# Performance work log

Hardware: AMD Instinct MI355X
Metric: run time of the kernel (lower is better)

## Reference

```python
import jax, jax.numpy as jnp
import numpy as np

N = 100000
E = 1600000
F_IN = 100
HID = 128
CLS = 47


def _glorot(key, shape):
    fan_in, fan_out = shape[1], shape[0]
    lim = (6.0 / (fan_in + fan_out)) ** 0.5
    return jax.random.uniform(key, shape, jnp.float32, -lim, lim)


def setup_inputs() -> dict:
    key = jax.random.key(0)
    ks = jax.random.split(key, 12)
    x0 = jax.random.normal(ks[0], (N, F_IN), jnp.float32)
    edge_index = jax.random.randint(ks[1], (2, E), 0, N, jnp.int32)
    edge_weight = jax.random.uniform(ks[2], (E,), jnp.float32)
    params = {
        'W1_rel': _glorot(ks[3], (HID, F_IN)),
        'W1_root': _glorot(ks[4], (HID, F_IN)),
        'b1': jnp.zeros((HID,), jnp.float32),
        'W2_rel': _glorot(ks[5], (HID, HID)),
        'W2_root': _glorot(ks[6], (HID, HID)),
        'b2': jnp.zeros((HID,), jnp.float32),
        'W3_rel': _glorot(ks[7], (HID, HID)),
        'W3_root': _glorot(ks[8], (HID, HID)),
        'b3': jnp.zeros((HID,), jnp.float32),
        'W_lin': _glorot(ks[9], (CLS, 3 * HID)),
        'b_lin': jnp.zeros((CLS,), jnp.float32),
    }
    return dict(x0=x0, edge_index=edge_index, edge_weight=edge_weight, **params)


def _graph_conv(x, src, dst, ew, W_rel, W_root, b):
    # gather source features, scale by edge weight, scatter-add to destinations
    msg = x[src] * ew[:, None]                       # [E, d]
    agg = jax.ops.segment_sum(msg, dst, num_segments=N)  # [N, d]
    return agg @ W_rel.T + x @ W_root.T + b


def reference(x0, edge_index, edge_weight,
              W1_rel, W1_root, b1,
              W2_rel, W2_root, b2,
              W3_rel, W3_root, b3,
              W_lin, b_lin):
    src, dst = edge_index[0], edge_index[1]
    x1 = jax.nn.relu(_graph_conv(x0, src, dst, edge_weight, W1_rel, W1_root, b1))
    x2 = jax.nn.relu(_graph_conv(x1, src, dst, edge_weight, W2_rel, W2_root, b2))
    x3 = jax.nn.relu(_graph_conv(x2, src, dst, edge_weight, W3_rel, W3_root, b3))
    x = jnp.concatenate([x1, x2, x3], axis=-1)       # [N, 3*HID]
    logits = x @ W_lin.T + b_lin                     # [N, CLS]
    return jax.nn.log_softmax(logits, axis=-1)
```

## Files before the change

### kernel.cpp

```cpp
#include <hip/hip_runtime.h>
#include <hip/hip_bf16.h>
#include <stdint.h>

#define NN 100000
#define NE 1600000
#define FIN 100
#define HID 128
#define CLS 47
#define NBUK 391
#define BCAP 4992

typedef __attribute__((ext_vector_type(8))) short bf16x8;
typedef __attribute__((ext_vector_type(4))) float f32x4;
typedef __attribute__((ext_vector_type(2))) float f32x2;

#define AS1(p) ((const __attribute__((address_space(1))) void*)(p))
#define AS3(p) ((__attribute__((address_space(3))) void*)(p))

__device__ __forceinline__ uint16_t f2bf(float f) {
  union { float f; uint32_t u; } v; v.f = f;
  uint32_t r = v.u + 0x7fffu + ((v.u >> 16) & 1u);
  return (uint16_t)(r >> 16);
}

__global__ void pack_weights(const float* __restrict__ W1r, const float* __restrict__ W1o,
                             const float* __restrict__ W2r, const float* __restrict__ W2o,
                             const float* __restrict__ W3r, const float* __restrict__ W3o,
                             uint16_t* __restrict__ B1, uint16_t* __restrict__ B2, uint16_t* __restrict__ B3) {
  int idx = blockIdx.x * 256 + threadIdx.x;
  int l = idx >> 15;
  int rem = idx & 32767;
  int j = rem >> 8;
  int k = rem & 255;
  if (l == 0) {
    uint16_t v = 0;
    if (k < FIN) v = f2bf(W1r[j*FIN + k]);
    else if (k >= 128 && k < 128 + FIN) v = f2bf(W1o[j*FIN + (k - 128)]);
    B1[j*256 + k] = v;
  } else if (l == 1) {
    B2[j*256 + k] = (k < 128) ? f2bf(W2r[j*128 + k]) : f2bf(W2o[j*128 + (k - 128)]);
  } else {
    B3[j*256 + k] = (k < 128) ? f2bf(W3r[j*128 + k]) : f2bf(W3o[j*128 + (k - 128)]);
  }
}

__global__ void pack_wl(const float* __restrict__ Wl, uint16_t* __restrict__ Wlb) {
  int idx = blockIdx.x * 256 + threadIdx.x;
  int r = idx / 384;
  int c = idx - r * 384;
  Wlb[idx] = (r < CLS) ? f2bf(Wl[r*384 + c]) : (uint16_t)0;
}

__global__ __launch_bounds__(256) void pad_x0(const float* __restrict__ x0, uint16_t* __restrict__ x0p,
                                              uint8_t* __restrict__ x0f8) {
  int n = blockIdx.x * 4 + (threadIdx.x >> 6);
  int c = 2 * (threadIdx.x & 63);
  uint32_t o = 0;
  uint16_t o8 = 0;
  if (c < FIN) {
    float2 v = *(const float2*)(x0 + (size_t)n*FIN + c);
    o = ((uint32_t)f2bf(v.y) << 16) | (uint32_t)f2bf(v.x);
    o8 = (uint16_t)__builtin_amdgcn_cvt_pk_fp8_f32(v.x, v.y, 0, false);
  }
  *(uint32_t*)(x0p + (size_t)n*HID + c) = o;
  *(uint16_t*)(x0f8 + (size_t)n*128 + c) = o8;
}

__global__ void binit(int* __restrict__ bfill) {
  int i = blockIdx.x * 256 + threadIdx.x;
  if (i < NBUK) bfill[i] = i * BCAP;
}

__global__ __launch_bounds__(512) void binscat(const int* __restrict__ src, const int* __restrict__ dst,
                                               const float* __restrict__ ew,
                                               int* __restrict__ bfill, int2* __restrict__ ebin) {
  __shared__ int h[NBUK];
  __shared__ int base[NBUK];
  int tid = threadIdx.x;
  for (int i = tid; i < NBUK; i += 512) h[i] = 0;
  __syncthreads();
  int tile0 = blockIdx.x * 8192;
  int n = NE - tile0; if (n > 8192) n = 8192;
  for (int i = tid; i < n; i += 512) atomicAdd(&h[dst[tile0 + i] >> 8], 1);
  __syncthreads();
  for (int i = tid; i < NBUK; i += 512) base[i] = h[i] ? atomicAdd(&bfill[i], h[i]) : 0;
  __syncthreads();
  for (int i = tid; i < NBUK; i += 512) h[i] = 0;
  __syncthreads();
  for (int i = tid; i < n; i += 512) {
    int e = tile0 + i;
    int d = dst[e];
    int b = d >> 8;
    int r = atomicAdd(&h[b], 1);
    ebin[base[b] + r] = make_int2(src[e] | ((d & 255) << 17), __float_as_int(ew[e]));
  }
}

__global__ __launch_bounds__(256) void bucket_csr(const int2* __restrict__ ebin,
                                                  const int* __restrict__ bfill,
                                                  int2* __restrict__ row_desc,
                                                  int2* __restrict__ erec) {
  __shared__ int sh[256];
  __shared__ int fill[256];
  __shared__ int cnt2s;
  int b = blockIdx.x;
  int tid = threadIdx.x;
  int base = b * BCAP;
  int cnt = bfill[b] - base;
  sh[tid] = 0;
  __syncthreads();
  for (int i = tid; i < cnt; i += 256) atomicAdd(&sh[(uint32_t)ebin[base + i].x >> 17], 1);
  __syncthreads();
  int histv = sh[tid];
  int hist2 = (histv + 1) & ~1;
  __syncthreads();
  sh[tid] = hist2;
  __syncthreads();
  for (int off = 1; off < 256; off <<= 1) {
    int tv = (tid >= off) ? sh[tid - off] : 0;
    __syncthreads();
    sh[tid] += tv;
    __syncthreads();
  }
  int excl2 = sh[tid] - hist2;
  if (tid == 255) cnt2s = sh[255];
  int node = b * 256 + tid;
  if (node < NN) row_desc[node] = make_int2(base + excl2, histv);
  fill[tid] = base + excl2;
  if (histv & 1) erec[base + excl2 + histv] = make_int2(0, 0);
  __syncthreads();
  for (int i = tid; i < cnt; i += 256) {
    int2 rec = ebin[base + i];
    int dl = (uint32_t)rec.x >> 17;
    int s = rec.x & 0x1FFFF;
    int pos = atomicAdd(&fill[dl], 1);
    erec[pos] = make_int2(s << 7, rec.y);
  }
  if (tid < 16) {
    int p = cnt2s + tid;
    if (p < BCAP) erec[base + p] = make_int2(0, 0);
  }
}

__global__ __launch_bounds__(256) void spmm_kernel(const uint8_t* __restrict__ x8,
                                                   const int2* __restrict__ row_desc,
                                                   const int2* __restrict__ erec,
                                                   uint16_t* __restrict__ agg) {
  int wave = threadIdx.x >> 6;
  int l = threadIdx.x & 63;
  int half = l >> 5, li = l & 31;
  int n = blockIdx.x * 8 + wave * 2 + half;
  int2 rd = row_desc[n];
  int s0 = rd.x, deg = rd.y;
  const char* xb = (const char*)x8;
  int loff = 4 * li;
  f32x2 a01 = (f32x2){0.f, 0.f}, a23 = (f32x2){0.f, 0.f};
  const int4* ep4 = (const int4*)(erec + s0);
  int nfull = deg & ~15;
  const int4* epf = ep4 + (nfull >> 1);
  for (; ep4 < epf; ep4 += 8) {
    int4 r[8];
    #pragma unroll
    for (int u = 0; u < 8; ++u) r[u] = ep4[u];
    uint32_t g[16];
    #pragma unroll
    for (int u = 0; u < 8; ++u) {
      g[2*u]   = *(const uint32_t*)(xb + (size_t)(uint32_t)(r[u].x + loff));
      g[2*u+1] = *(const uint32_t*)(xb + (size_t)(uint32_t)(r[u].z + loff));
    }
    __builtin_amdgcn_sched_barrier(0);
    #pragma unroll
    for (int u = 0; u < 8; ++u) {
      float w0 = __int_as_float(r[u].y);
      float w1 = __int_as_float(r[u].w);
      f32x2 w20 = (f32x2){w0, w0}, w21 = (f32x2){w1, w1};
      a01 += w20 * __builtin_amdgcn_cvt_pk_f32_fp8(g[2*u], false);
      a23 += w20 * __builtin_amdgcn_cvt_pk_f32_fp8(g[2*u], true);
      a01 += w21 * __builtin_amdgcn_cvt_pk_f32_fp8(g[2*u+1], false);
      a23 += w21 * __builtin_amdgcn_cvt_pk_f32_fp8(g[2*u+1], true);
    }
  }
  int rem = deg - nfull;
  if (rem) {
    int4 r[8];
    #pragma unroll
    for (int u = 0; u < 8; ++u) r[u] = ep4[u];
    uint32_t g[16];
    #pragma unroll
    for (int u = 0; u < 8; ++u) {
      g[2*u]   = *(const uint32_t*)(xb + (size_t)(uint32_t)(r[u].x + loff));
      g[2*u+1] = *(const uint32_t*)(xb + (size_t)(uint32_t)(r[u].z + loff));
    }
    __builtin_amdgcn_sched_barrier(0);
    #pragma unroll
    for (int u = 0; u < 8; ++u) {
      float w0 = (2*u     < rem) ? __int_as_float(r[u].y) : 0.f;
      float w1 = (2*u + 1 < rem) ? __int_as_float(r[u].w) : 0.f;
      f32x2 w20 = (f32x2){w0, w0}, w21 = (f32x2){w1, w1};
      a01 += w20 * __builtin_amdgcn_cvt_pk_f32_fp8(g[2*u], false);
      a23 += w20 * __builtin_amdgcn_cvt_pk_f32_fp8(g[2*u], true);
      a01 += w21 * __builtin_amdgcn_cvt_pk_f32_fp8(g[2*u+1], false);
      a23 += w21 * __builtin_amdgcn_cvt_pk_f32_fp8(g[2*u+1], true);
    }
  }
  uint2 o;
  o.x = ((uint32_t)f2bf(a01[1]) << 16) | (uint32_t)f2bf(a01[0]);
  o.y = ((uint32_t)f2bf(a23[1]) << 16) | (uint32_t)f2bf(a23[0]);
  *(uint2*)(agg + (size_t)n*HID + 4*li) = o;
}

__global__ __launch_bounds__(256) void gemm_kernel(const uint16_t* __restrict__ A1, const uint16_t* __restrict__ A2,
                                                   const uint16_t* __restrict__ Bm, const float* __restrict__ bias,
                                                   uint16_t* __restrict__ out, uint8_t* __restrict__ out8) {
  __shared__ uint16_t ldsA[64 * 32];
  __shared__ uint16_t ldsB[128 * 32];
  int t = threadIdx.x;
  int n0 = blockIdx.x * 64;
  int lane = t & 63, wave = t >> 6;
  int wm = (wave >> 1) * 32;
  int wn = (wave & 1) * 64;
  int l15 = lane & 15, quad = lane >> 4;

  f32x4 acc[2][4];
  #pragma unroll
  for (int i = 0; i < 2; ++i)
    #pragma unroll
    for (int j = 0; j < 4; ++j) acc[i][j] = (f32x4){0.f, 0.f, 0.f, 0.f};

  int ra = t >> 2, qa = t & 3;
  int qsA = (qa + (ra >> 1)) & 3;
  int rowA = n0 + ra; if (rowA >= NN) rowA = NN - 1;

  for (int kt = 0; kt < 8; ++kt) {
    int kbase = kt * 32;
    const uint16_t* Asrc = (kbase < 128) ? A1 : A2;
    int klocal = kbase & 127;
    __builtin_amdgcn_global_load_lds(AS1(Asrc + (size_t)rowA*HID + klocal + qsA*8), AS3(&ldsA[t * 8]), 16, 0, 0);
    #pragma unroll
    for (int p = 0; p < 2; ++p) {
      int u = t + p * 256;
      int j = u >> 2, qb = u & 3;
      int qsB = (qb + (j >> 1)) & 3;
      __builtin_amdgcn_global_load_lds(AS1(Bm + j*256 + kbase + qsB*8), AS3(&ldsB[u * 8]), 16, 0, 0);
    }
    __syncthreads();
    bf16x8 af[2], bfr[4];
    #pragma unroll
    for (int mi = 0; mi < 2; ++mi) {
      int rA = wm + mi*16 + l15;
      af[mi] = *(const bf16x8*)&ldsA[rA * 32 + ((quad - (rA >> 1)) & 3) * 8];
    }
    #pragma unroll
    for (int ni = 0; ni < 4; ++ni) {
      int j = wn + ni*16 + l15;
      bfr[ni] = *(const bf16x8*)&ldsB[j * 32 + ((quad - (j >> 1)) & 3) * 8];
    }
    #pragma unroll
    for (int mi = 0; mi < 2; ++mi)
      #pragma unroll
      for (int ni = 0; ni < 4; ++ni)
        acc[mi][ni] = __builtin_amdgcn_mfma_f32_16x16x32_bf16(af[mi], bfr[ni], acc[mi][ni], 0, 0, 0);
    __syncthreads();
  }

  #pragma unroll
  for (int mi = 0; mi < 2; ++mi) {
    #pragma unroll
    for (int ni = 0; ni < 4; ++ni) {
      int c = wn + ni*16 + l15;
      float bc = bias[c];
      #pragma unroll
      for (int i = 0; i < 4; ++i) {
        int r = n0 + wm + mi*16 + quad*4 + i;
        if (r < NN) {
          float v = acc[mi][ni][i] + bc;
          v = v > 0.f ? v : 0.f;
          out[(size_t)r*HID + c] = f2bf(v);
          if (out8) out8[(size_t)r*128 + c] = (uint8_t)__builtin_amdgcn_cvt_pk_fp8_f32(v, v, 0, false);
        }
      }
    }
  }
}

__global__ __launch_bounds__(256) void final_kernel(const uint16_t* __restrict__ x1, const uint16_t* __restrict__ x2,
                                                    const uint16_t* __restrict__ x3,
                                                    const uint16_t* __restrict__ Wlb, const float* __restrict__ bl,
                                                    float* __restrict__ out) {
  __shared__ uint16_t ldsA[64 * 16 * 8];
  __shared__ uint16_t ldsW[64 * 16 * 8];
  int t = threadIdx.x;
  int lane = t & 63, wave = t >> 6;
  int n0 = blockIdx.x * 64;
  int l15 = lane & 15, quad = lane >> 4;

  f32x4 acc[3];
  #pragma unroll
  for (int i = 0; i < 3; ++i) acc[i] = (f32x4){0.f, 0.f, 0.f, 0.f};

  #pragma unroll
  for (int rr = 0; rr < 3; ++rr) {
    const uint16_t* xs = (rr == 0) ? x1 : (rr == 1) ? x2 : x3;
    #pragma unroll
    for (int q = 0; q < 4; ++q) {
      int u = t + q * 256;
      int row = u >> 4, cp = u & 15;
      int c = cp ^ (row & 15);
      int rowA = n0 + row; if (rowA >= NN) rowA = NN - 1;
      __builtin_amdgcn_global_load_lds(AS1(xs + (size_t)rowA*HID + c*8), AS3(&ldsA[u * 8]), 16, 0, 0);
      int rowW = row < 48 ? row : 47;
      __builtin_amdgcn_global_load_lds(AS1(Wlb + (size_t)rowW*384 + rr*128 + c*8), AS3(&ldsW[u * 8]), 16, 0, 0);
    }
    __syncthreads();
    #pragma unroll
    for (int kt = 0; kt < 4; ++kt) {
      int cA = kt * 4 + quad;
      int rA = wave * 16 + l15;
      bf16x8 af = *(const bf16x8*)&ldsA[(rA * 16 + (cA ^ (rA & 15))) * 8];
      #pragma unroll
      for (int nt = 0; nt < 3; ++nt) {
        int rW = nt * 16 + l15;
        bf16x8 wf = *(const bf16x8*)&ldsW[(rW * 16 + (cA ^ (rW & 15))) * 8];
        acc[nt] = __builtin_amdgcn_mfma_f32_16x16x32_bf16(af, wf, acc[nt], 0, 0, 0);
      }
    }
    __syncthreads();
  }

  int nb = n0 + wave * 16;
  float bias[3]; bool valid[3];
  #pragma unroll
  for (int nt = 0; nt < 3; ++nt) {
    int c = nt*16 + l15;
    valid[nt] = (c < CLS);
    bias[nt] = valid[nt] ? bl[c] : 0.f;
  }

  #pragma unroll
  for (int i = 0; i < 4; ++i) {
    int r = nb + quad*4 + i;
    float v0 = acc[0][i] + bias[0];
    float v1 = acc[1][i] + bias[1];
    float v2 = valid[2] ? (acc[2][i] + bias[2]) : -INFINITY;
    float m = fmaxf(v0, fmaxf(v1, v2));
    #pragma unroll
    for (int off = 8; off >= 1; off >>= 1) m = fmaxf(m, __shfl_xor(m, off, 64));
    float s = __expf(v0 - m) + __expf(v1 - m) + (valid[2] ? __expf(v2 - m) : 0.f);
    #pragma unroll
    for (int off = 8; off >= 1; off >>= 1) s += __shfl_xor(s, off, 64);
    float lse = m + __logf(s);
    if (r < NN) {
      out[(size_t)r*CLS + l15]      = v0 - lse;
      out[(size_t)r*CLS + 16 + l15] = v1 - lse;
      if (valid[2]) out[(size_t)r*CLS + 32 + l15] = v2 - lse;
    }
  }
}

extern "C" void kernel_launch(void* const* d_in, const int* in_sizes, int n_in,
                              void* d_out, int out_size, void* d_ws, size_t ws_size,
                              hipStream_t stream) {
  (void)in_sizes; (void)n_in; (void)out_size; (void)ws_size;
  const float* x0  = (const float*)d_in[0];
  const int*   ei  = (const int*)d_in[1];
  const float* ew  = (const float*)d_in[2];
  const float* W1r = (const float*)d_in[3];
  const float* W1o = (const float*)d_in[4];
  const float* b1  = (const float*)d_in[5];
  const float* W2r = (const float*)d_in[6];
  const float* W2o = (const float*)d_in[7];
  const float* b2  = (const float*)d_in[8];
  const float* W3r = (const float*)d_in[9];
  const float* W3o = (const float*)d_in[10];
  const float* b3  = (const float*)d_in[11];
  const float* Wl  = (const float*)d_in[12];
  const float* bl  = (const float*)d_in[13];
  const int* src = ei;
  const int* dst = ei + NE;

  char* ws = (char*)d_ws;
  size_t off = 0;
  auto alloc = [&](size_t bytes) -> void* {
    void* p = ws + off;
    off += (bytes + 255) & ~(size_t)255;
    return p;
  };
  uint16_t* x0p = (uint16_t*)alloc((size_t)NN * HID * 2);
  uint16_t* xb1 = (uint16_t*)alloc((size_t)NN * HID * 2);
  uint16_t* xb3 = (uint16_t*)alloc((size_t)NN * HID * 2);
  uint16_t* agg = (uint16_t*)alloc((size_t)NN * HID * 2);
  int2*   erec      = (int2*)alloc((size_t)NBUK * BCAP * 8);
  int2*   ebin      = (int2*)alloc((size_t)NBUK * BCAP * 8);
  int2*   row_desc  = (int2*)alloc((size_t)NN * 8);
  int*    bfill     = (int*)alloc(NBUK * 4);
  uint16_t* B1 = (uint16_t*)alloc(128 * 256 * 2);
  uint16_t* B2 = (uint16_t*)alloc(128 * 256 * 2);
  uint16_t* B3 = (uint16_t*)alloc(128 * 256 * 2);
  uint16_t* Wlb = (uint16_t*)alloc(48 * 384 * 2);
  uint8_t* x0f8  = (uint8_t*)alloc((size_t)NN * 128);
  uint8_t* xb2f8 = (uint8_t*)alloc((size_t)NN * 128);
  uint16_t* xb2 = x0p;
  uint8_t* xb1f8 = (uint8_t*)ebin;

  const int TB = (NE + 8191) / 8192;

  binit<<<2, 256, 0, stream>>>(bfill);
  pack_weights<<<384, 256, 0, stream>>>(W1r, W1o, W2r, W2o, W3r, W3o, B1, B2, B3);
  pack_wl<<<72, 256, 0, stream>>>(Wl, Wlb);
  pad_x0<<<NN / 4, 256, 0, stream>>>(x0, x0p, x0f8);
  binscat<<<TB, 512, 0, stream>>>(src, dst, ew, bfill, ebin);
  bucket_csr<<<NBUK, 256, 0, stream>>>(ebin, bfill, row_desc, erec);

  spmm_kernel<<<NN / 8, 256, 0, stream>>>(x0f8, row_desc, erec, agg);
  gemm_kernel<<<(NN + 63) / 64, 256, 0, stream>>>(agg, x0p, B1, b1, xb1, xb1f8);
  spmm_kernel<<<NN / 8, 256, 0, stream>>>(xb1f8, row_desc, erec, agg);
  gemm_kernel<<<(NN + 63) / 64, 256, 0, stream>>>(agg, xb1, B2, b2, xb2, xb2f8);
  spmm_kernel<<<NN / 8, 256, 0, stream>>>(xb2f8, row_desc, erec, agg);
  gemm_kernel<<<(NN + 63) / 64, 256, 0, stream>>>(agg, xb2, B3, b3, xb3, nullptr);

  final_kernel<<<(NN + 63) / 64, 256, 0, stream>>>(xb1, xb2, xb3, Wlb, bl, (float*)d_out);
}
```

Measured before the change: 381.5 us.

## Fuse SpMM aggregation into GEMM via shared-memory aggregate tile

Each GEMM block now computes the SpMM aggregation for its 64 rows itself and stores the bf16 result in an XOR-swizzled LDS tile. The first half of the K loop reads that tile directly instead of loading an agg buffer from global memory. This removes the global agg round trip and three kernel launches per forward pass. In exchange, each block uses more LDS, which may lower occupancy, and the gather phase is serialized before the MFMA phase inside each block.

New measurement: 434.7 us. 1.14x slower.

```diff
diff --git a/kernel.cpp b/kernel.cpp
--- a/kernel.cpp
+++ b/kernel.cpp
@@ -142,81 +142,87 @@
   }
 }
 
-__global__ __launch_bounds__(256) void spmm_kernel(const uint8_t* __restrict__ x8,
-                                                   const int2* __restrict__ row_desc,
-                                                   const int2* __restrict__ erec,
-                                                   uint16_t* __restrict__ agg) {
-  int wave = threadIdx.x >> 6;
-  int l = threadIdx.x & 63;
-  int half = l >> 5, li = l & 31;
-  int n = blockIdx.x * 8 + wave * 2 + half;
-  int2 rd = row_desc[n];
-  int s0 = rd.x, deg = rd.y;
-  const char* xb = (const char*)x8;
-  int loff = 4 * li;
-  f32x2 a01 = (f32x2){0.f, 0.f}, a23 = (f32x2){0.f, 0.f};
-  const int4* ep4 = (const int4*)(erec + s0);
-  int nfull = deg & ~15;
-  const int4* epf = ep4 + (nfull >> 1);
-  for (; ep4 < epf; ep4 += 8) {
-    int4 r[8];
-    #pragma unroll
-    for (int u = 0; u < 8; ++u) r[u] = ep4[u];
-    uint32_t g[16];
-    #pragma unroll
-    for (int u = 0; u < 8; ++u) {
-      g[2*u]   = *(const uint32_t*)(xb + (size_t)(uint32_t)(r[u].x + loff));
-      g[2*u+1] = *(const uint32_t*)(xb + (size_t)(uint32_t)(r[u].z + loff));
-    }
-    __builtin_amdgcn_sched_barrier(0);
-    #pragma unroll
-    for (int u = 0; u < 8; ++u) {
-      float w0 = __int_as_float(r[u].y);
-      float w1 = __int_as_float(r[u].w);
-      f32x2 w20 = (f32x2){w0, w0}, w21 = (f32x2){w1, w1};
-      a01 += w20 * __builtin_amdgcn_cvt_pk_f32_fp8(g[2*u], false);
-      a23 += w20 * __builtin_amdgcn_cvt_pk_f32_fp8(g[2*u], true);
-      a01 += w21 * __builtin_amdgcn_cvt_pk_f32_fp8(g[2*u+1], false);
-      a23 += w21 * __builtin_amdgcn_cvt_pk_f32_fp8(g[2*u+1], true);
-    }
-  }
-  int rem = deg - nfull;
-  if (rem) {
-    int4 r[8];
-    #pragma unroll
-    for (int u = 0; u < 8; ++u) r[u] = ep4[u];
-    uint32_t g[16];
-    #pragma unroll
-    for (int u = 0; u < 8; ++u) {
-      g[2*u]   = *(const uint32_t*)(xb + (size_t)(uint32_t)(r[u].x + loff));
-      g[2*u+1] = *(const uint32_t*)(xb + (size_t)(uint32_t)(r[u].z + loff));
-    }
-    __builtin_amdgcn_sched_barrier(0);
-    #pragma unroll
-    for (int u = 0; u < 8; ++u) {
-      float w0 = (2*u     < rem) ? __int_as_float(r[u].y) : 0.f;
-      float w1 = (2*u + 1 < rem) ? __int_as_float(r[u].w) : 0.f;
-      f32x2 w20 = (f32x2){w0, w0}, w21 = (f32x2){w1, w1};
-      a01 += w20 * __builtin_amdgcn_cvt_pk_f32_fp8(g[2*u], false);
-      a23 += w20 * __builtin_amdgcn_cvt_pk_f32_fp8(g[2*u], true);
-      a01 += w21 * __builtin_amdgcn_cvt_pk_f32_fp8(g[2*u+1], false);
-      a23 += w21 * __builtin_amdgcn_cvt_pk_f32_fp8(g[2*u+1], true);
-    }
-  }
-  uint2 o;
-  o.x = ((uint32_t)f2bf(a01[1]) << 16) | (uint32_t)f2bf(a01[0]);
-  o.y = ((uint32_t)f2bf(a23[1]) << 16) | (uint32_t)f2bf(a23[0]);
-  *(uint2*)(agg + (size_t)n*HID + 4*li) = o;
-}
-
-__global__ __launch_bounds__(256) void gemm_kernel(const uint16_t* __restrict__ A1, const uint16_t* __restrict__ A2,
-                                                   const uint16_t* __restrict__ Bm, const float* __restrict__ bias,
-                                                   uint16_t* __restrict__ out, uint8_t* __restrict__ out8) {
+__global__ __launch_bounds__(256) void spmm_gemm_kernel(
+    const uint8_t* __restrict__ x8,
+    const int2* __restrict__ row_desc,
+    const int2* __restrict__ erec,
+    const uint16_t* __restrict__ Xr,
+    const uint16_t* __restrict__ Bm,
+    const float* __restrict__ bias,
+    uint16_t* __restrict__ out, uint8_t* __restrict__ out8) {
+  __shared__ uint16_t ldsAgg[64 * 128];
   __shared__ uint16_t ldsA[64 * 32];
   __shared__ uint16_t ldsB[128 * 32];
   int t = threadIdx.x;
   int n0 = blockIdx.x * 64;
   int lane = t & 63, wave = t >> 6;
+  int half = lane >> 5, li = lane & 31;
+
+  const char* xb = (const char*)x8;
+  int loff = 4 * li;
+  for (int it = 0; it < 8; ++it) {
+    int rloc = wave * 16 + 2 * it + half;
+    int n = n0 + rloc;
+    int s0 = 0, deg = 0;
+    if (n < NN) { int2 rd = row_desc[n]; s0 = rd.x; deg = rd.y; }
+    f32x2 a01 = (f32x2){0.f, 0.f}, a23 = (f32x2){0.f, 0.f};
+    const int4* ep4 = (const int4*)(erec + s0);
+    int nfull = deg & ~15;
+    const int4* epf = ep4 + (nfull >> 1);
+    for (; ep4 < epf; ep4 += 8) {
+      int4 r[8];
+      #pragma unroll
+      for (int u = 0; u < 8; ++u) r[u] = ep4[u];
+      uint32_t g[16];
+      #pragma unroll
+      for (int u = 0; u < 8; ++u) {
+        g[2*u]   = *(const uint32_t*)(xb + (size_t)(uint32_t)(r[u].x + loff));
+        g[2*u+1] = *(const uint32_t*)(xb + (size_t)(uint32_t)(r[u].z + loff));
+      }
+      __builtin_amdgcn_sched_barrier(0);
+      #pragma unroll
+      for (int u = 0; u < 8; ++u) {
+        float w0 = __int_as_float(r[u].y);
+        float w1 = __int_as_float(r[u].w);
+        f32x2 w20 = (f32x2){w0, w0}, w21 = (f32x2){w1, w1};
+        a01 += w20 * __builtin_amdgcn_cvt_pk_f32_fp8(g[2*u], false);
+        a23 += w20 * __builtin_amdgcn_cvt_pk_f32_fp8(g[2*u], true);
+        a01 += w21 * __builtin_amdgcn_cvt_pk_f32_fp8(g[2*u+1], false);
+        a23 += w21 * __builtin_amdgcn_cvt_pk_f32_fp8(g[2*u+1], true);
+      }
+    }
+    int rem = deg - nfull;
+    if (rem) {
+      int4 r[8];
+      #pragma unroll
+      for (int u = 0; u < 8; ++u) r[u] = ep4[u];
+      uint32_t g[16];
+      #pragma unroll
+      for (int u = 0; u < 8; ++u) {
+        g[2*u]   = *(const uint32_t*)(xb + (size_t)(uint32_t)(r[u].x + loff));
+        g[2*u+1] = *(const uint32_t*)(xb + (size_t)(uint32_t)(r[u].z + loff));
+      }
+      __builtin_amdgcn_sched_barrier(0);
+      #pragma unroll
+      for (int u = 0; u < 8; ++u) {
+        float w0 = (2*u     < rem) ? __int_as_float(r[u].y) : 0.f;
+        float w1 = (2*u + 1 < rem) ? __int_as_float(r[u].w) : 0.f;
+        f32x2 w20 = (f32x2){w0, w0}, w21 = (f32x2){w1, w1};
+        a01 += w20 * __builtin_amdgcn_cvt_pk_f32_fp8(g[2*u], false);
+        a23 += w20 * __builtin_amdgcn_cvt_pk_f32_fp8(g[2*u], true);
+        a01 += w21 * __builtin_amdgcn_cvt_pk_f32_fp8(g[2*u+1], false);
+        a23 += w21 * __builtin_amdgcn_cvt_pk_f32_fp8(g[2*u+1], true);
+      }
+    }
+    uint2 o;
+    o.x = ((uint32_t)f2bf(a01[1]) << 16) | (uint32_t)f2bf(a01[0]);
+    o.y = ((uint32_t)f2bf(a23[1]) << 16) | (uint32_t)f2bf(a23[0]);
+    int ci = li >> 1;
+    int cs = ci ^ (rloc & 15);
+    *(uint2*)&ldsAgg[rloc * 128 + cs * 8 + (li & 1) * 4] = o;
+  }
+  __syncthreads();
+
   int wm = (wave >> 1) * 32;
   int wn = (wave & 1) * 64;
   int l15 = lane & 15, quad = lane >> 4;
@@ -233,9 +239,8 @@
 
   for (int kt = 0; kt < 8; ++kt) {
     int kbase = kt * 32;
-    const uint16_t* Asrc = (kbase < 128) ? A1 : A2;
-    int klocal = kbase & 127;
-    __builtin_amdgcn_global_load_lds(AS1(Asrc + (size_t)rowA*HID + klocal + qsA*8), AS3(&ldsA[t * 8]), 16, 0, 0);
+    if (kt >= 4)
+      __builtin_amdgcn_global_load_lds(AS1(Xr + (size_t)rowA*HID + (kbase - 128) + qsA*8), AS3(&ldsA[t * 8]), 16, 0, 0);
     #pragma unroll
     for (int p = 0; p < 2; ++p) {
       int u = t + p * 256;
@@ -248,7 +253,12 @@
     #pragma unroll
     for (int mi = 0; mi < 2; ++mi) {
       int rA = wm + mi*16 + l15;
-      af[mi] = *(const bf16x8*)&ldsA[rA * 32 + ((quad - (rA >> 1)) & 3) * 8];
+      if (kt < 4) {
+        int ci = kt * 4 + quad;
+        af[mi] = *(const bf16x8*)&ldsAgg[rA * 128 + (ci ^ (rA & 15)) * 8];
+      } else {
+        af[mi] = *(const bf16x8*)&ldsA[rA * 32 + ((quad - (rA >> 1)) & 3) * 8];
+      }
     }
     #pragma unroll
     for (int ni = 0; ni < 4; ++ni) {
@@ -388,7 +398,6 @@
   uint16_t* x0p = (uint16_t*)alloc((size_t)NN * HID * 2);
   uint16_t* xb1 = (uint16_t*)alloc((size_t)NN * HID * 2);
   uint16_t* xb3 = (uint16_t*)alloc((size_t)NN * HID * 2);
-  uint16_t* agg = (uint16_t*)alloc((size_t)NN * HID * 2);
   int2*   erec      = (int2*)alloc((size_t)NBUK * BCAP * 8);
   int2*   ebin      = (int2*)alloc((size_t)NBUK * BCAP * 8);
   int2*   row_desc  = (int2*)alloc((size_t)NN * 8);
@@ -411,12 +420,9 @@
   binscat<<<TB, 512, 0, stream>>>(src, dst, ew, bfill, ebin);
   bucket_csr<<<NBUK, 256, 0, stream>>>(ebin, bfill, row_desc, erec);
 
-  spmm_kernel<<<NN / 8, 256, 0, stream>>>(x0f8, row_desc, erec, agg);
-  gemm_kernel<<<(NN + 63) / 64, 256, 0, stream>>>(agg, x0p, B1, b1, xb1, xb1f8);
-  spmm_kernel<<<NN / 8, 256, 0, stream>>>(xb1f8, row_desc, erec, agg);
-  gemm_kernel<<<(NN + 63) / 64, 256, 0, stream>>>(agg, xb1, B2, b2, xb2, xb2f8);
-  spmm_kernel<<<NN / 8, 256, 0, stream>>>(xb2f8, row_desc, erec, agg);
-  gemm_kernel<<<(NN + 63) / 64, 256, 0, stream>>>(agg, xb2, B3, b3, xb3, nullptr);
+  spmm_gemm_kernel<<<(NN + 63) / 64, 256, 0, stream>>>(x0f8, row_desc, erec, x0p, B1, b1, xb1, xb1f8);
+  spmm_gemm_kernel<<<(NN + 63) / 64, 256, 0, stream>>>(xb1f8, row_desc, erec, xb1, B2, b2, xb2, xb2f8);
+  spmm_gemm_kernel<<<(NN + 63) / 64, 256, 0, stream>>>(xb2f8, row_desc, erec, xb2, B3, b3, xb3, nullptr);
 
   final_kernel<<<(NN + 63) / 64, 256, 0, stream>>>(xb1, xb2, xb3, Wlb, bl, (float*)d_out);
 }
```
